# Kernel tuning notes

Hardware: AMD Instinct MI355X
Metric: run time of the kernel (lower is better)

Reference implementation:

```python
import jax, jax.numpy as jnp
import numpy as np

V, D, H, L, S, B, HD, FF, MAXS = 50257, 1024, 8, 6, 1024, 2, 128, 4096, 2048
EPS = 1e-5
STD = 0.02


def rmsnorm(x, w):
    rms = jnp.sqrt(jnp.mean(x * x, axis=-1, keepdims=True) + EPS)
    return w * (x / rms)


def setup_inputs() -> dict:
    key = jax.random.key(0)
    ks = jax.random.split(key, 9)
    return {
        "tokens": jax.random.randint(ks[0], (S, B), 0, V),
        "tok_emb": STD * jax.random.normal(ks[1], (V, D), jnp.float32),
        "pos_emb": STD * jax.random.normal(ks[2], (MAXS, D), jnp.float32),
        "attn_norm_w": jnp.ones((L, D), jnp.float32),
        "Wq": STD * jax.random.normal(ks[3], (L, H, D, HD), jnp.float32),
        "Wk": STD * jax.random.normal(ks[4], (L, H, D, HD), jnp.float32),
        "Wv": STD * jax.random.normal(ks[5], (L, H, D, HD), jnp.float32),
        "Wo": STD * jax.random.normal(ks[6], (L, H, HD, D), jnp.float32),
        "mlp_norm_w": jnp.ones((L, D), jnp.float32),
        "W1": STD * jax.random.normal(ks[7], (L, D, FF), jnp.float32),
        "W2": STD * jax.random.normal(ks[8], (L, FF, D), jnp.float32),
        "final_norm_w": jnp.ones((D,), jnp.float32),
    }


def reference(tokens, tok_emb, pos_emb, attn_norm_w, Wq, Wk, Wv, Wo,
              mlp_norm_w, W1, W2, final_norm_w):
    seq_len = tokens.shape[0]
    scale = HD ** -0.5
    # (S, B, D) token + learned positional embeddings
    x = tok_emb[tokens] + pos_emb[:seq_len][:, None, :]
    causal = jnp.tril(jnp.ones((seq_len, seq_len), bool))  # (S, S)
    for l in range(L):
        n = rmsnorm(x, attn_norm_w[l])
        q = jnp.einsum('sbd,hdk->bhsk', n, Wq[l])
        k = jnp.einsum('sbd,hdk->bhsk', n, Wk[l])
        v = jnp.einsum('sbd,hdk->bhsk', n, Wv[l])
        scores = jnp.einsum('bhsk,bhtk->bhst', q, k) * scale
        scores = jnp.where(causal, scores, -jnp.inf)
        w = jax.nn.softmax(scores, axis=-1)
        attn = jnp.einsum('bhst,bhtk->bhsk', w, v)
        # per-head out_proj summed over heads (matches sum over head modules)
        x = x + jnp.einsum('bhsk,hkd->sbd', attn, Wo[l])
        m = rmsnorm(x, mlp_norm_w[l])
        h = jax.nn.silu(jnp.einsum('sbd,df->sbf', m, W1[l]))
        x = x + jnp.einsum('sbf,fd->sbd', h, W2[l])
    x = rmsnorm(x, final_norm_w)
    logits = jnp.einsum('sbd,vd->sbv', x, tok_emb)  # tied lm_head
    return logits
```

## Files before the change

### kernel.cpp

```cpp
#include <hip/hip_runtime.h>
#include <hip/hip_bf16.h>
#include <cstddef>
#include <cstdint>

#define VOCAB 50257
#define VPAD  50432
#define DMODEL 1024
#define NHEAD 8
#define NLAYER 6
#define SEQ 1024
#define BATCH 2
#define HDIM 128
#define FFDIM 4096
#define NTOK (SEQ * BATCH)
#define QKVLD 3072
#define EPSV 1e-5f


typedef __attribute__((ext_vector_type(8))) short short8;
typedef __attribute__((ext_vector_type(4))) float f32x4;

__device__ __forceinline__ unsigned short f2bf(float f) {
    union { float f; unsigned u; } v; v.f = f;
    unsigned r = v.u + 0x7FFF + ((v.u >> 16) & 1);
    return (unsigned short)(r >> 16);
}

__global__ __launch_bounds__(256) void embed_kernel(
    const int* __restrict__ tokens, const float* __restrict__ tok_emb,
    const float* __restrict__ pos_emb, float* __restrict__ x)
{
    int idx = blockIdx.x * 256 + threadIdx.x;
    int t = idx >> 10;
    int d = idx & (DMODEL - 1);
    int b = t >> 10, s = t & (SEQ - 1);
    int tok = tokens[s * BATCH + b];
    x[idx] = tok_emb[(size_t)tok * DMODEL + d] + pos_emb[(size_t)s * DMODEL + d];
}

__global__ __launch_bounds__(256) void rmsnorm_bf_kernel(
    const float* __restrict__ x, const float* __restrict__ w,
    unsigned short* __restrict__ o)
{
    int t = blockIdx.x;
    int tid = threadIdx.x;
    const float4 xv = ((const float4*)(x + (size_t)t * DMODEL))[tid];
    float ss = xv.x * xv.x + xv.y * xv.y + xv.z * xv.z + xv.w * xv.w;
    __shared__ float red[256];
    red[tid] = ss;
    __syncthreads();
    for (int off = 128; off > 0; off >>= 1) {
        if (tid < off) red[tid] += red[tid + off];
        __syncthreads();
    }
    float inv = rsqrtf(red[0] * (1.0f / DMODEL) + EPSV);
    const float4 wv = ((const float4*)w)[tid];
    ushort4 ov;
    ov.x = f2bf(wv.x * xv.x * inv);
    ov.y = f2bf(wv.y * xv.y * inv);
    ov.z = f2bf(wv.z * xv.z * inv);
    ov.w = f2bf(wv.w * xv.w * inv);
    ((ushort4*)(o + (size_t)t * DMODEL))[tid] = ov;
}

__global__ __launch_bounds__(256) void transpose_cast_kernel(
    const float* __restrict__ in, unsigned short* __restrict__ out, int R, int C)
{
    __shared__ float tile[32][33];
    const size_t bo = (size_t)blockIdx.z * R * C;
    const float* src = in + bo;
    unsigned short* dst = out + bo;
    int c0 = blockIdx.x * 32, r0 = blockIdx.y * 32;
    int tx = threadIdx.x, ty = threadIdx.y;
    #pragma unroll
    for (int i = 0; i < 32; i += 8)
        tile[ty + i][tx] = src[(size_t)(r0 + ty + i) * C + c0 + tx];
    __syncthreads();
    #pragma unroll
    for (int i = 0; i < 32; i += 8)
        dst[(size_t)(c0 + ty + i) * R + r0 + tx] = f2bf(tile[tx][ty + i]);
}

__global__ __launch_bounds__(256) void transpose_qkv_kernel(
    const float* __restrict__ in, unsigned short* __restrict__ out, int row_off)
{
    __shared__ float tile[32][33];
    int z = blockIdx.z;
    int l = z >> 3, h = z & 7;
    const float* src = in + (size_t)z * DMODEL * HDIM;
    unsigned short* dst = out + (size_t)l * QKVLD * DMODEL
                              + (size_t)(row_off + h * HDIM) * DMODEL;
    int c0 = blockIdx.x * 32, r0 = blockIdx.y * 32;
    int tx = threadIdx.x, ty = threadIdx.y;
    #pragma unroll
    for (int i = 0; i < 32; i += 8)
        tile[ty + i][tx] = src[(size_t)(r0 + ty + i) * HDIM + c0 + tx];
    __syncthreads();
    #pragma unroll
    for (int i = 0; i < 32; i += 8)
        dst[(size_t)(c0 + ty + i) * DMODEL + r0 + tx] = f2bf(tile[tx][ty + i]);
}

__global__ __launch_bounds__(256) void vt_transpose_kernel(
    const unsigned short* __restrict__ qkv, unsigned short* __restrict__ vt)
{
    __shared__ unsigned short tile[32][33];
    int c0 = blockIdx.x * 32;
    int r0 = blockIdx.y * 32;
    int tx = threadIdx.x, ty = threadIdx.y;
    #pragma unroll
    for (int i = 0; i < 32; i += 8)
        tile[ty + i][tx] = qkv[(size_t)(r0 + ty + i) * QKVLD + 2048 + c0 + tx];
    __syncthreads();
    #pragma unroll
    for (int i = 0; i < 32; i += 8)
        vt[(size_t)(c0 + ty + i) * NTOK + r0 + tx] = tile[tx][ty + i];
}

__global__ __launch_bounds__(256) void cast_pad_kernel(
    const float* __restrict__ in, unsigned short* __restrict__ out,
    long n_src, long n_tot)
{
    long i = ((long)blockIdx.x * 256 + threadIdx.x) * 8;
    if (i >= n_tot) return;
    short8 o8;
    if (i < n_src) {
        const float4* p = (const float4*)(in + i);
        float4 a = p[0], b = p[1];
        o8[0] = (short)f2bf(a.x); o8[1] = (short)f2bf(a.y);
        o8[2] = (short)f2bf(a.z); o8[3] = (short)f2bf(a.w);
        o8[4] = (short)f2bf(b.x); o8[5] = (short)f2bf(b.y);
        o8[6] = (short)f2bf(b.z); o8[7] = (short)f2bf(b.w);
    } else {
        o8 = (short8)0;
    }
    *(short8*)(out + i) = o8;
}

template<bool ATOMIC, bool SILU, bool BF16OUT, int RM>
__global__ __launch_bounds__(256, 2) void mm128_kernel(
    const unsigned short* __restrict__ A, const unsigned short* __restrict__ Bt,
    void* __restrict__ Cv, int M, int N, int K, int rows, int ksplit)
{
    int nwg = gridDim.x;
    int flat = blockIdx.x;
    int q8 = nwg >> 3, r8 = nwg & 7;
    int xcd = flat & 7, lid = flat >> 3;
    int wg = (r8 == 0) ? (xcd * q8 + lid)
           : ((xcd < r8 ? xcd * (q8 + 1) : r8 * (q8 + 1) + (xcd - r8) * q8) + lid);
    int rs = rows * ksplit;
    const int col0 = (wg / rs) * 128;
    int rem = wg % rs;
    const int row0 = (rem / ksplit) * 128;
    const int sk   = rem % ksplit;
    const int Keff = K / ksplit;
    const int kbase = sk * Keff;

    __shared__ __align__(16) char lds[65536];
    const int tid  = threadIdx.x;
    const int lane = tid & 63;
    const int wave = tid >> 6;
    const int wm = wave >> 1, wn = wave & 1;
    const int g  = lane >> 4;
    const int c  = lane & 15;

    f32x4 acc[4][4] = {};

    auto STAGE = [&](int buf, int t) {
        const int k0 = kbase + t * 32;
        char* base = lds + buf * 16384;
        #pragma unroll
        for (int j = 0; j < 2; ++j) {
            int chunk = j * 256 + tid;
            int row = chunk >> 2, slot = chunk & 3;
            int ss = slot ^ ((row >> 1) & 3);
            __builtin_amdgcn_global_load_lds(
                (const __attribute__((address_space(1))) void*)
                    (A + (size_t)(row0 + row) * K + k0 + ss * 8),
                (__attribute__((address_space(3))) void*)(base + chunk * 16), 16, 0, 0);
        }
        #pragma unroll
        for (int j = 0; j < 2; ++j) {
            int chunk = j * 256 + tid;
            int row = chunk >> 2, slot = chunk & 3;
            int ss = slot ^ ((row >> 1) & 3);
            __builtin_amdgcn_global_load_lds(
                (const __attribute__((address_space(1))) void*)
                    (Bt + (size_t)(col0 + row) * K + k0 + ss * 8),
                (__attribute__((address_space(3))) void*)(base + 8192 + chunk * 16), 16, 0, 0);
        }
    };

    const int NT = Keff >> 5;
    STAGE(0, 0);
    if (NT > 1) STAGE(1, 1);
    if (NT > 2) STAGE(2, 2);
    if (NT > 2)      asm volatile("s_waitcnt vmcnt(8)" ::: "memory");
    else if (NT > 1) asm volatile("s_waitcnt vmcnt(4)" ::: "memory");
    else             asm volatile("s_waitcnt vmcnt(0)" ::: "memory");
    __builtin_amdgcn_s_barrier();
    __builtin_amdgcn_sched_barrier(0);

    for (int t = 0; t < NT; ++t) {
        if (t + 3 < NT) STAGE((t + 3) & 3, t + 3);

        char* base = lds + (t & 3) * 16384;
        short8 af[4], bf[4];
        #pragma unroll
        for (int i = 0; i < 4; ++i) {
            int rowa = wm * 64 + i * 16 + c;
            af[i] = *(const short8*)(base + rowa * 64 + ((g ^ ((rowa >> 1) & 3)) << 4));
            int rowb = wn * 64 + i * 16 + c;
            bf[i] = *(const short8*)(base + 8192 + rowb * 64 + ((g ^ ((rowb >> 1) & 3)) << 4));
        }
        __builtin_amdgcn_s_setprio(1);
        #pragma unroll
        for (int i = 0; i < 4; ++i)
            #pragma unroll
            for (int j = 0; j < 4; ++j)
                acc[i][j] = __builtin_amdgcn_mfma_f32_16x16x32_bf16(
                    af[i], bf[j], acc[i][j], 0, 0, 0);
        __builtin_amdgcn_s_setprio(0);
        __builtin_amdgcn_sched_barrier(0);

        if (t + 1 < NT) {
            if (t + 3 < NT)      asm volatile("s_waitcnt vmcnt(8)" ::: "memory");
            else if (t + 2 < NT) asm volatile("s_waitcnt vmcnt(4)" ::: "memory");
            else                 asm volatile("s_waitcnt vmcnt(0)" ::: "memory");
            __builtin_amdgcn_s_barrier();
            __builtin_amdgcn_sched_barrier(0);
        }
    }

    float* Cf = (float*)Cv;
    unsigned short* Cb = (unsigned short*)Cv;
    const int crow  = row0 + wm * 64 + g * 4;
    const int ccol0 = col0 + wn * 64 + c;
    #pragma unroll
    for (int i = 0; i < 4; ++i) {
        #pragma unroll
        for (int j = 0; j < 4; ++j) {
            int gcol = ccol0 + j * 16;
            if (gcol < N) {
                #pragma unroll
                for (int r = 0; r < 4; ++r) {
                    int grow = crow + i * 16 + r;
                    int orow = RM ? (((grow & (SEQ - 1)) << 1) | (grow >> 10)) : grow;
                    float v = acc[i][j][r];
                    if (SILU) v = v / (1.0f + __expf(-v));
                    size_t ci = (size_t)orow * N + gcol;
                    if (ATOMIC)       atomicAdd(&Cf[ci], v);
                    else if (BF16OUT) Cb[ci] = f2bf(v);
                    else              Cf[ci] = v;
                }
            }
        }
    }
}

template<bool SILU, bool BF16OUT, int RM>
__global__ __launch_bounds__(512, 1) void mm256_kernel(
    const unsigned short* __restrict__ A, const unsigned short* __restrict__ Bt,
    void* __restrict__ Cv, int M, int N, int K, int rows)
{
    int nwg = gridDim.x;
    int flat = blockIdx.x;
    int q8 = nwg >> 3, r8 = nwg & 7;
    int xcd = flat & 7, lid = flat >> 3;
    int wg = (r8 == 0) ? (xcd * q8 + lid)
           : ((xcd < r8 ? xcd * (q8 + 1) : r8 * (q8 + 1) + (xcd - r8) * q8) + lid);
    const int row0 = (wg % rows) * 256;
    const int col0 = (wg / rows) * 256;

    __shared__ __align__(16) char lds[131072];
    const int tid  = threadIdx.x;
    const int lane = tid & 63;
    const int wave = tid >> 6;
    const int wm = wave >> 2;
    const int wn = wave & 3;
    const int g  = lane >> 4;
    const int c  = lane & 15;

    f32x4 acc[8][4] = {};

    auto STAGE = [&](int buf, int tile) {
        const int k0 = tile * 32;
        char* base = lds + buf * 32768;
        #pragma unroll
        for (int j = 0; j < 2; ++j) {
            int chunk = j * 512 + tid;
            int row = chunk >> 2, slot = chunk & 3;
            int sslot = slot ^ ((row >> 1) & 3);
            __builtin_amdgcn_global_load_lds(
                (const __attribute__((address_space(1))) void*)
                    (A + (size_t)(row0 + row) * K + k0 + sslot * 8),
                (__attribute__((address_space(3))) void*)(base + chunk * 16), 16, 0, 0);
        }
        #pragma unroll
        for (int j = 0; j < 2; ++j) {
            int chunk = j * 512 + tid;
            int row = chunk >> 2, slot = chunk & 3;
            int sslot = slot ^ ((row >> 1) & 3);
            __builtin_amdgcn_global_load_lds(
                (const __attribute__((address_space(1))) void*)
                    (Bt + (size_t)(col0 + row) * K + k0 + sslot * 8),
                (__attribute__((address_space(3))) void*)(base + 16384 + chunk * 16), 16, 0, 0);
        }
    };

    const int NT = K >> 5;
    STAGE(0, 0); STAGE(1, 1); STAGE(2, 2);
    asm volatile("s_waitcnt vmcnt(8)" ::: "memory");
    __builtin_amdgcn_s_barrier();
    __builtin_amdgcn_sched_barrier(0);

    for (int t = 0; t < NT; ++t) {
        if (t + 3 < NT) STAGE((t + 3) & 3, t + 3);

        char* base = lds + (t & 3) * 32768;
        short8 af[8], bf[4];
        #pragma unroll
        for (int mf = 0; mf < 8; ++mf) {
            int row = wm * 128 + mf * 16 + c;
            af[mf] = *(const short8*)(base + row * 64 + ((g ^ ((row >> 1) & 3)) << 4));
        }
        #pragma unroll
        for (int nf = 0; nf < 4; ++nf) {
            int row = wn * 64 + nf * 16 + c;
            bf[nf] = *(const short8*)(base + 16384 + row * 64 + ((g ^ ((row >> 1) & 3)) << 4));
        }
        __builtin_amdgcn_s_setprio(1);
        #pragma unroll
        for (int mf = 0; mf < 8; ++mf)
            #pragma unroll
            for (int nf = 0; nf < 4; ++nf)
                acc[mf][nf] = __builtin_amdgcn_mfma_f32_16x16x32_bf16(
                    af[mf], bf[nf], acc[mf][nf], 0, 0, 0);
        __builtin_amdgcn_s_setprio(0);
        __builtin_amdgcn_sched_barrier(0);

        if (t + 1 < NT) {
            if (t + 3 < NT)      asm volatile("s_waitcnt vmcnt(8)" ::: "memory");
            else if (t + 2 < NT) asm volatile("s_waitcnt vmcnt(4)" ::: "memory");
            else                 asm volatile("s_waitcnt vmcnt(0)" ::: "memory");
            __builtin_amdgcn_s_barrier();
            __builtin_amdgcn_sched_barrier(0);
        }
    }

    float* Cf = (float*)Cv;
    unsigned short* Cb = (unsigned short*)Cv;
    #pragma unroll
    for (int mf = 0; mf < 8; ++mf) {
        #pragma unroll
        for (int nf = 0; nf < 4; ++nf) {
            int gcol = col0 + wn * 64 + nf * 16 + c;
            if (gcol < N) {
                #pragma unroll
                for (int r = 0; r < 4; ++r) {
                    int grow = row0 + wm * 128 + mf * 16 + g * 4 + r;
                    int orow = RM ? (((grow & (SEQ - 1)) << 1) | (grow >> 10)) : grow;
                    float v = acc[mf][nf][r];
                    if (SILU) v = v / (1.0f + __expf(-v));
                    size_t ci = (size_t)orow * N + gcol;
                    if (BF16OUT) Cb[ci] = f2bf(v);
                    else         Cf[ci] = v;
                }
            }
        }
    }
}

__global__ __launch_bounds__(256) void flash_attn_kernel(
    const unsigned short* __restrict__ q, const unsigned short* __restrict__ k,
    const unsigned short* __restrict__ vt, unsigned short* __restrict__ o)
{
    const int qt   = blockIdx.x;
    const int h    = blockIdx.y;
    const int b    = blockIdx.z;
    const int tid  = threadIdx.x;
    const int lane = tid & 63;
    const int wave = tid >> 6;
    const int g    = lane >> 4;
    const int c    = lane & 15;

    __shared__ unsigned short k_lds[64 * 128];
    __shared__ unsigned short vt_lds[128 * 64];
    __shared__ unsigned short p_lds[4 * 16 * 64];

    const int q0  = qt * 64;
    const int wq0 = q0 + wave * 16;
    const int tokb = b * SEQ;

    short8 qf[4];
    {
        const unsigned short* qr =
            q + (size_t)(tokb + wq0 + c) * QKVLD + h * HDIM + g * 8;
        #pragma unroll
        for (int dblk = 0; dblk < 4; ++dblk)
            qf[dblk] = *(const short8*)(qr + dblk * 32);
    }

    f32x4 oacc[8] = {};
    float m = -1e30f, l = 0.f;
    const float scale = 0.08838834764831845f;
    const int myq = wq0 + c;

    const int nt = qt + 1;
    for (int it = 0; it < nt; ++it) {
        const int kv0 = it * 64;
        short8 kc[4], vc[4];
        #pragma unroll
        for (int i = 0; i < 4; ++i) {
            int chunk = tid + i * 256;
            int key = chunk >> 4, cc = chunk & 15;
            kc[i] = *(const short8*)(
                k + (size_t)(tokb + kv0 + key) * QKVLD + h * HDIM + cc * 8);
        }
        #pragma unroll
        for (int i = 0; i < 4; ++i) {
            int chunk = tid + i * 256;
            int d = chunk >> 3, cc = chunk & 7;
            vc[i] = *(const short8*)(
                vt + (size_t)(h * HDIM + d) * NTOK + tokb + kv0 + cc * 8);
        }
        __syncthreads();
        #pragma unroll
        for (int i = 0; i < 4; ++i) {
            int chunk = tid + i * 256;
            int key = chunk >> 4, cc = chunk & 15;
            *(short8*)((char*)k_lds + ((key * 256 + cc * 16) ^ ((key & 7) << 4))) = kc[i];
        }
        #pragma unroll
        for (int i = 0; i < 4; ++i) {
            int chunk = tid + i * 256;
            int d = chunk >> 3, cc = chunk & 7;
            *(short8*)((char*)vt_lds + ((d * 128 + cc * 16) ^ ((d & 7) << 4))) = vc[i];
        }
        __syncthreads();

        f32x4 st[4];
        #pragma unroll
        for (int sub = 0; sub < 4; ++sub) {
            f32x4 acc = {};
            int key = sub * 16 + c;
            #pragma unroll
            for (int dblk = 0; dblk < 4; ++dblk) {
                short8 kf = *(const short8*)((char*)k_lds +
                    ((key * 256 + dblk * 64 + g * 16) ^ ((key & 7) << 4)));
                acc = __builtin_amdgcn_mfma_f32_16x16x32_bf16(kf, qf[dblk], acc, 0, 0, 0);
            }
            st[sub] = acc;
        }

        #pragma unroll
        for (int sub = 0; sub < 4; ++sub)
            #pragma unroll
            for (int r = 0; r < 4; ++r) {
                int key = kv0 + sub * 16 + g * 4 + r;
                float s = st[sub][r] * scale;
                st[sub][r] = (key <= myq) ? s : -1e30f;
            }

        float tm = -1e30f;
        #pragma unroll
        for (int sub = 0; sub < 4; ++sub)
            #pragma unroll
            for (int r = 0; r < 4; ++r) tm = fmaxf(tm, st[sub][r]);
        tm = fmaxf(tm, __shfl_xor(tm, 16));
        tm = fmaxf(tm, __shfl_xor(tm, 32));
        float mnew = fmaxf(m, tm);
        float sc_f = __expf(m - mnew);
        m = mnew;

        float ps = 0.f;
        #pragma unroll
        for (int sub = 0; sub < 4; ++sub) {
            float p0 = __expf(st[sub][0] - m);
            float p1 = __expf(st[sub][1] - m);
            float p2 = __expf(st[sub][2] - m);
            float p3 = __expf(st[sub][3] - m);
            ps += (p0 + p1) + (p2 + p3);
            ushort4 pk;
            pk.x = f2bf(p0); pk.y = f2bf(p1); pk.z = f2bf(p2); pk.w = f2bf(p3);
            *(ushort4*)((char*)p_lds + wave * 2048 +
                ((c * 128 + sub * 32 + g * 8) ^ ((c & 7) << 4))) = pk;
        }
        ps += __shfl_xor(ps, 16);
        ps += __shfl_xor(ps, 32);
        l = l * sc_f + ps;
        #pragma unroll
        for (int dt = 0; dt < 8; ++dt)
            #pragma unroll
            for (int r = 0; r < 4; ++r) oacc[dt][r] *= sc_f;

        #pragma unroll
        for (int kb = 0; kb < 2; ++kb) {
            short8 pf = *(const short8*)((char*)p_lds + wave * 2048 +
                ((c * 128 + kb * 64 + g * 16) ^ ((c & 7) << 4)));
            #pragma unroll
            for (int dt = 0; dt < 8; ++dt) {
                int d = dt * 16 + c;
                short8 vf = *(const short8*)((char*)vt_lds +
                    ((d * 128 + kb * 64 + g * 16) ^ ((d & 7) << 4)));
                oacc[dt] = __builtin_amdgcn_mfma_f32_16x16x32_bf16(vf, pf, oacc[dt], 0, 0, 0);
            }
        }
    }

    float inv = 1.0f / l;
    unsigned short* orow = o + (size_t)(tokb + wq0 + c) * DMODEL + h * HDIM + g * 4;
    #pragma unroll
    for (int dt = 0; dt < 8; ++dt) {
        ushort4 ov;
        ov.x = f2bf(oacc[dt][0] * inv);
        ov.y = f2bf(oacc[dt][1] * inv);
        ov.z = f2bf(oacc[dt][2] * inv);
        ov.w = f2bf(oacc[dt][3] * inv);
        *(ushort4*)(orow + dt * 16) = ov;
    }
}

extern "C" void kernel_launch(void* const* d_in, const int* in_sizes, int n_in,
                              void* d_out, int out_size, void* d_ws, size_t ws_size,
                              hipStream_t stream)
{
    const int*   tokens       = (const int*)  d_in[0];
    const float* tok_emb      = (const float*)d_in[1];
    const float* pos_emb      = (const float*)d_in[2];
    const float* attn_norm_w  = (const float*)d_in[3];
    const float* Wq           = (const float*)d_in[4];
    const float* Wk           = (const float*)d_in[5];
    const float* Wv           = (const float*)d_in[6];
    const float* Wo           = (const float*)d_in[7];
    const float* mlp_norm_w   = (const float*)d_in[8];
    const float* W1           = (const float*)d_in[9];
    const float* W2           = (const float*)d_in[10];
    const float* final_norm_w = (const float*)d_in[11];
    float* out = (float*)d_out;

    char* wp = (char*)d_ws;
    size_t off = 0;
    auto alloc = [&](size_t bytes) -> void* {
        void* p = wp + off;
        off += (bytes + 255) & ~(size_t)255;
        return p;
    };
    float* x             = (float*)alloc((size_t)NTOK * DMODEL * 4);
    unsigned short* nbf     = (unsigned short*)alloc((size_t)NTOK * DMODEL * 2);
    unsigned short* qkvbf   = (unsigned short*)alloc((size_t)NTOK * QKVLD * 2);
    unsigned short* vtb     = (unsigned short*)alloc((size_t)DMODEL * NTOK * 2);
    unsigned short* attnbf  = (unsigned short*)alloc((size_t)NTOK * DMODEL * 2);
    unsigned short* hbf     = (unsigned short*)alloc((size_t)NTOK * FFDIM * 2);
    unsigned short* temb    = (unsigned short*)alloc((size_t)VPAD * DMODEL * 2);
    unsigned short* Wqkv_t  = (unsigned short*)alloc((size_t)NLAYER * QKVLD * DMODEL * 2);
    unsigned short* Wo_t    = (unsigned short*)alloc((size_t)NLAYER * DMODEL * DMODEL * 2);
    unsigned short* W1_t    = (unsigned short*)alloc((size_t)NLAYER * DMODEL * FFDIM * 2);
    unsigned short* W2_t    = (unsigned short*)alloc((size_t)NLAYER * FFDIM * DMODEL * 2);
    if (off > ws_size) return;

    {
        dim3 bb(32, 8), g(HDIM / 32, DMODEL / 32, NLAYER * NHEAD);
        transpose_qkv_kernel<<<g, bb, 0, stream>>>(Wq, Wqkv_t, 0);
        transpose_qkv_kernel<<<g, bb, 0, stream>>>(Wk, Wqkv_t, DMODEL);
        transpose_qkv_kernel<<<g, bb, 0, stream>>>(Wv, Wqkv_t, 2 * DMODEL);
    }
    {
        dim3 bb(32, 8), g(DMODEL / 32, DMODEL / 32, NLAYER);
        transpose_cast_kernel<<<g, bb, 0, stream>>>(Wo, Wo_t, DMODEL, DMODEL);
    }
    {
        dim3 bb(32, 8), g(FFDIM / 32, DMODEL / 32, NLAYER);
        transpose_cast_kernel<<<g, bb, 0, stream>>>(W1, W1_t, DMODEL, FFDIM);
    }
    {
        dim3 bb(32, 8), g(DMODEL / 32, FFDIM / 32, NLAYER);
        transpose_cast_kernel<<<g, bb, 0, stream>>>(W2, W2_t, FFDIM, DMODEL);
    }
    {
        long n_src = (long)VOCAB * DMODEL, n_tot = (long)VPAD * DMODEL;
        cast_pad_kernel<<<(unsigned)(n_tot / 8 / 256), 256, 0, stream>>>(
            tok_emb, temb, n_src, n_tot);
    }

    embed_kernel<<<(NTOK * DMODEL) / 256, 256, 0, stream>>>(tokens, tok_emb, pos_emb, x);

    const size_t LW    = (size_t)DMODEL * DMODEL;
    const size_t LWQKV = (size_t)QKVLD * DMODEL;
    const size_t LWF   = (size_t)DMODEL * FFDIM;

    for (int l = 0; l < NLAYER; l++) {
        rmsnorm_bf_kernel<<<NTOK, 256, 0, stream>>>(x, attn_norm_w + (size_t)l * DMODEL, nbf);
        mm128_kernel<false, false, true, 0><<<384, 256, 0, stream>>>(
            nbf, Wqkv_t + l * LWQKV, qkvbf, NTOK, QKVLD, DMODEL, 16, 1);
        vt_transpose_kernel<<<dim3(DMODEL / 32, NTOK / 32), dim3(32, 8), 0, stream>>>(
            qkvbf, vtb);
        flash_attn_kernel<<<dim3(SEQ / 64, NHEAD, BATCH), 256, 0, stream>>>(
            qkvbf, qkvbf + DMODEL, vtb, attnbf);
        mm128_kernel<true, false, false, 0><<<8 * 16 * 2, 256, 0, stream>>>(
            attnbf, Wo_t + l * LW, x, NTOK, DMODEL, DMODEL, 16, 2);
        rmsnorm_bf_kernel<<<NTOK, 256, 0, stream>>>(x, mlp_norm_w + (size_t)l * DMODEL, nbf);
        mm128_kernel<false, true, true, 0><<<32 * 16, 256, 0, stream>>>(
            nbf, W1_t + l * LWF, hbf, NTOK, FFDIM, DMODEL, 16, 1);
        mm128_kernel<true, false, false, 0><<<8 * 16 * 2, 256, 0, stream>>>(
            hbf, W2_t + l * LWF, x, NTOK, DMODEL, FFDIM, 16, 2);
    }

    rmsnorm_bf_kernel<<<NTOK, 256, 0, stream>>>(x, final_norm_w, nbf);
    mm256_kernel<false, false, 1><<<8 * 197, 512, 0, stream>>>(
        nbf, temb, out, NTOK, VOCAB, DMODEL, 8);
}
```

Measured before the change: 1.415 ms.

## Restructure lm_head GEMM into ping-pong half-tile staging pipeline

Rewrites the 256x256 lm_head GEMM main loop to use 64-wide K tiles split into four quarter-stages with two LDS buffers. Each global-to-LDS load for an operand half is issued between MFMA sub-blocks, and barriers are placed around each compute phase. The goal is to interleave memory loads more finely with matrix math and to read fewer fragments into registers at a time. The cost is more barriers per iteration and a more intricate wait-count schedule, which risks stalls or races if the counts are wrong.

After: 1.427 ms. Within noise of the previous version (+0.9%).

```diff
diff --git a/kernel.cpp b/kernel.cpp
--- a/kernel.cpp
+++ b/kernel.cpp
@@ -259,7 +259,7 @@
 }
 
 template<bool SILU, bool BF16OUT, int RM>
-__global__ __launch_bounds__(512, 1) void mm256_kernel(
+__global__ __launch_bounds__(512, 1) void mm256p_kernel(
     const unsigned short* __restrict__ A, const unsigned short* __restrict__ Bt,
     void* __restrict__ Cv, int M, int N, int K, int rows)
 {
@@ -283,69 +283,104 @@
 
     f32x4 acc[8][4] = {};
 
-    auto STAGE = [&](int buf, int tile) {
-        const int k0 = tile * 32;
-        char* base = lds + buf * 32768;
+    auto STAGE = [&](int buf, int op, int ks, int tile) {
+        char* base = lds + (buf << 16) + (op << 15) + (ks << 14);
+        const unsigned short* src =
+            (op ? Bt + (size_t)col0 * K : A + (size_t)row0 * K) + tile * 64 + ks * 32;
         #pragma unroll
         for (int j = 0; j < 2; ++j) {
             int chunk = j * 512 + tid;
             int row = chunk >> 2, slot = chunk & 3;
-            int sslot = slot ^ ((row >> 1) & 3);
+            int ss = slot ^ ((row >> 1) & 3);
             __builtin_amdgcn_global_load_lds(
                 (const __attribute__((address_space(1))) void*)
-                    (A + (size_t)(row0 + row) * K + k0 + sslot * 8),
+                    (src + (size_t)row * K + ss * 8),
                 (__attribute__((address_space(3))) void*)(base + chunk * 16), 16, 0, 0);
         }
-        #pragma unroll
-        for (int j = 0; j < 2; ++j) {
-            int chunk = j * 512 + tid;
-            int row = chunk >> 2, slot = chunk & 3;
-            int sslot = slot ^ ((row >> 1) & 3);
-            __builtin_amdgcn_global_load_lds(
-                (const __attribute__((address_space(1))) void*)
-                    (Bt + (size_t)(col0 + row) * K + k0 + sslot * 8),
-                (__attribute__((address_space(3))) void*)(base + 16384 + chunk * 16), 16, 0, 0);
-        }
     };
-
-    const int NT = K >> 5;
-    STAGE(0, 0); STAGE(1, 1); STAGE(2, 2);
-    asm volatile("s_waitcnt vmcnt(8)" ::: "memory");
+    auto RD = [&](int buf, int op, int ks, int row) -> short8 {
+        char* base = lds + (buf << 16) + (op << 15) + (ks << 14);
+        return *(const short8*)(base + row * 64 + ((g ^ ((row >> 1) & 3)) << 4));
+    };
+
+    const int NT = K >> 6;
+    STAGE(0, 1, 0, 0); STAGE(0, 0, 0, 0); STAGE(0, 1, 1, 0); STAGE(0, 0, 1, 0);
+    STAGE(1, 1, 0, 1); STAGE(1, 0, 0, 1); STAGE(1, 1, 1, 1);
+    asm volatile("s_waitcnt vmcnt(6)" ::: "memory");
     __builtin_amdgcn_s_barrier();
     __builtin_amdgcn_sched_barrier(0);
 
-    for (int t = 0; t < NT; ++t) {
-        if (t + 3 < NT) STAGE((t + 3) & 3, t + 3);
-
-        char* base = lds + (t & 3) * 32768;
-        short8 af[8], bf[4];
-        #pragma unroll
-        for (int mf = 0; mf < 8; ++mf) {
-            int row = wm * 128 + mf * 16 + c;
-            af[mf] = *(const short8*)(base + row * 64 + ((g ^ ((row >> 1) & 3)) << 4));
-        }
-        #pragma unroll
-        for (int nf = 0; nf < 4; ++nf) {
-            int row = wn * 64 + nf * 16 + c;
-            bf[nf] = *(const short8*)(base + 16384 + row * 64 + ((g ^ ((row >> 1) & 3)) << 4));
-        }
+    for (int T = 0; T < NT; ++T) {
+        const int buf = T & 1;
+        short8 af[4], bf[4];
+
+        #pragma unroll
+        for (int i = 0; i < 4; ++i) af[i] = RD(buf, 0, 0, wm * 128 + i * 16 + c);
+        #pragma unroll
+        for (int j = 0; j < 4; ++j) bf[j] = RD(buf, 1, 0, wn * 64 + j * 16 + c);
+        if (T + 1 < NT) STAGE(buf ^ 1, 0, 1, T + 1);
+        __builtin_amdgcn_s_barrier();
         __builtin_amdgcn_s_setprio(1);
         #pragma unroll
-        for (int mf = 0; mf < 8; ++mf)
-            #pragma unroll
-            for (int nf = 0; nf < 4; ++nf)
-                acc[mf][nf] = __builtin_amdgcn_mfma_f32_16x16x32_bf16(
-                    af[mf], bf[nf], acc[mf][nf], 0, 0, 0);
+        for (int i = 0; i < 4; ++i)
+            #pragma unroll
+            for (int j = 0; j < 4; ++j)
+                acc[i][j] = __builtin_amdgcn_mfma_f32_16x16x32_bf16(
+                    af[i], bf[j], acc[i][j], 0, 0, 0);
         __builtin_amdgcn_s_setprio(0);
+        __builtin_amdgcn_s_barrier();
         __builtin_amdgcn_sched_barrier(0);
 
-        if (t + 1 < NT) {
-            if (t + 3 < NT)      asm volatile("s_waitcnt vmcnt(8)" ::: "memory");
-            else if (t + 2 < NT) asm volatile("s_waitcnt vmcnt(4)" ::: "memory");
-            else                 asm volatile("s_waitcnt vmcnt(0)" ::: "memory");
+        #pragma unroll
+        for (int i = 0; i < 4; ++i) af[i] = RD(buf, 0, 0, wm * 128 + 64 + i * 16 + c);
+        if (T + 2 < NT) STAGE(buf, 1, 0, T + 2);
+        __builtin_amdgcn_s_barrier();
+        __builtin_amdgcn_s_setprio(1);
+        #pragma unroll
+        for (int i = 0; i < 4; ++i)
+            #pragma unroll
+            for (int j = 0; j < 4; ++j)
+                acc[4 + i][j] = __builtin_amdgcn_mfma_f32_16x16x32_bf16(
+                    af[i], bf[j], acc[4 + i][j], 0, 0, 0);
+        __builtin_amdgcn_s_setprio(0);
+        __builtin_amdgcn_s_barrier();
+        __builtin_amdgcn_sched_barrier(0);
+
+        #pragma unroll
+        for (int i = 0; i < 4; ++i) af[i] = RD(buf, 0, 1, wm * 128 + i * 16 + c);
+        #pragma unroll
+        for (int j = 0; j < 4; ++j) bf[j] = RD(buf, 1, 1, wn * 64 + j * 16 + c);
+        if (T + 2 < NT) STAGE(buf, 0, 0, T + 2);
+        __builtin_amdgcn_s_barrier();
+        __builtin_amdgcn_s_setprio(1);
+        #pragma unroll
+        for (int i = 0; i < 4; ++i)
+            #pragma unroll
+            for (int j = 0; j < 4; ++j)
+                acc[i][j] = __builtin_amdgcn_mfma_f32_16x16x32_bf16(
+                    af[i], bf[j], acc[i][j], 0, 0, 0);
+        __builtin_amdgcn_s_setprio(0);
+        __builtin_amdgcn_s_barrier();
+        __builtin_amdgcn_sched_barrier(0);
+
+        #pragma unroll
+        for (int i = 0; i < 4; ++i) af[i] = RD(buf, 0, 1, wm * 128 + 64 + i * 16 + c);
+        if (T + 2 < NT) STAGE(buf, 1, 1, T + 2);
+        __builtin_amdgcn_s_barrier();
+        __builtin_amdgcn_s_setprio(1);
+        #pragma unroll
+        for (int i = 0; i < 4; ++i)
+            #pragma unroll
+            for (int j = 0; j < 4; ++j)
+                acc[4 + i][j] = __builtin_amdgcn_mfma_f32_16x16x32_bf16(
+                    af[i], bf[j], acc[4 + i][j], 0, 0, 0);
+        __builtin_amdgcn_s_setprio(0);
+        if (T + 1 < NT) {
+            if (T + 2 < NT) asm volatile("s_waitcnt vmcnt(6)" ::: "memory");
+            else            asm volatile("s_waitcnt vmcnt(0)" ::: "memory");
             __builtin_amdgcn_s_barrier();
-            __builtin_amdgcn_sched_barrier(0);
-        }
+        }
+        __builtin_amdgcn_sched_barrier(0);
     }
 
     float* Cf = (float*)Cv;
@@ -607,6 +642,6 @@
     }
 
     rmsnorm_bf_kernel<<<NTOK, 256, 0, stream>>>(x, final_norm_w, nbf);
-    mm256_kernel<false, false, 1><<<8 * 197, 512, 0, stream>>>(
+    mm256p_kernel<false, false, 1><<<8 * 197, 512, 0, stream>>>(
         nbf, temb, out, NTOK, VOCAB, DMODEL, 8);
 }
```

## Fuse V-transpose into QKV GEMM epilogue and use wave-per-row RMSNorm

Applied to the files above, without the earlier changes.

The QKV projection GEMM now writes the V columns straight into the transposed V buffer from its epilogue, which removes the separate vt_transpose kernel launch and its extra read and write of V. RMSNorm is rewritten so each wavefront handles one token row and reduces with cross-lane shuffles instead of an LDS tree with repeated barriers. The transposed V stores are strided by NTOK and uncoalesced, so the GEMM epilogue may get slower. Both changes are small next to the GEMMs and attention.

Result: slower. 1.458 ms (+3.1%).

```diff
diff --git a/kernel.cpp b/kernel.cpp
--- a/kernel.cpp
+++ b/kernel.cpp
@@ -42,25 +42,32 @@
     const float* __restrict__ x, const float* __restrict__ w,
     unsigned short* __restrict__ o)
 {
-    int t = blockIdx.x;
-    int tid = threadIdx.x;
-    const float4 xv = ((const float4*)(x + (size_t)t * DMODEL))[tid];
-    float ss = xv.x * xv.x + xv.y * xv.y + xv.z * xv.z + xv.w * xv.w;
-    __shared__ float red[256];
-    red[tid] = ss;
-    __syncthreads();
-    for (int off = 128; off > 0; off >>= 1) {
-        if (tid < off) red[tid] += red[tid + off];
-        __syncthreads();
-    }
-    float inv = rsqrtf(red[0] * (1.0f / DMODEL) + EPSV);
-    const float4 wv = ((const float4*)w)[tid];
-    ushort4 ov;
-    ov.x = f2bf(wv.x * xv.x * inv);
-    ov.y = f2bf(wv.y * xv.y * inv);
-    ov.z = f2bf(wv.z * xv.z * inv);
-    ov.w = f2bf(wv.w * xv.w * inv);
-    ((ushort4*)(o + (size_t)t * DMODEL))[tid] = ov;
+    const int wave = threadIdx.x >> 6, lane = threadIdx.x & 63;
+    const int t = blockIdx.x * 4 + wave;
+    const float4* xr = (const float4*)(x + (size_t)t * DMODEL);
+    const float4* wr = (const float4*)w;
+    float4 xv[4];
+    float ss = 0.f;
+    #pragma unroll
+    for (int j = 0; j < 4; ++j) {
+        xv[j] = xr[lane + 64 * j];
+        ss += xv[j].x * xv[j].x + xv[j].y * xv[j].y
+            + xv[j].z * xv[j].z + xv[j].w * xv[j].w;
+    }
+    #pragma unroll
+    for (int off = 1; off < 64; off <<= 1) ss += __shfl_xor(ss, off);
+    float inv = rsqrtf(ss * (1.0f / DMODEL) + EPSV);
+    ushort4* orow = (ushort4*)(o + (size_t)t * DMODEL);
+    #pragma unroll
+    for (int j = 0; j < 4; ++j) {
+        float4 wv = wr[lane + 64 * j];
+        ushort4 ov;
+        ov.x = f2bf(wv.x * xv[j].x * inv);
+        ov.y = f2bf(wv.y * xv[j].y * inv);
+        ov.z = f2bf(wv.z * xv[j].z * inv);
+        ov.w = f2bf(wv.w * xv[j].w * inv);
+        orow[lane + 64 * j] = ov;
+    }
 }
 
 __global__ __launch_bounds__(256) void transpose_cast_kernel(
@@ -99,22 +106,6 @@
     #pragma unroll
     for (int i = 0; i < 32; i += 8)
         dst[(size_t)(c0 + ty + i) * DMODEL + r0 + tx] = f2bf(tile[tx][ty + i]);
-}
-
-__global__ __launch_bounds__(256) void vt_transpose_kernel(
-    const unsigned short* __restrict__ qkv, unsigned short* __restrict__ vt)
-{
-    __shared__ unsigned short tile[32][33];
-    int c0 = blockIdx.x * 32;
-    int r0 = blockIdx.y * 32;
-    int tx = threadIdx.x, ty = threadIdx.y;
-    #pragma unroll
-    for (int i = 0; i < 32; i += 8)
-        tile[ty + i][tx] = qkv[(size_t)(r0 + ty + i) * QKVLD + 2048 + c0 + tx];
-    __syncthreads();
-    #pragma unroll
-    for (int i = 0; i < 32; i += 8)
-        vt[(size_t)(c0 + ty + i) * NTOK + r0 + tx] = tile[tx][ty + i];
 }
 
 __global__ __launch_bounds__(256) void cast_pad_kernel(
@@ -137,10 +128,11 @@
     *(short8*)(out + i) = o8;
 }
 
-template<bool ATOMIC, bool SILU, bool BF16OUT, int RM>
+template<bool ATOMIC, bool SILU, bool BF16OUT, int RM, int VT>
 __global__ __launch_bounds__(256, 2) void mm128_kernel(
     const unsigned short* __restrict__ A, const unsigned short* __restrict__ Bt,
-    void* __restrict__ Cv, int M, int N, int K, int rows, int ksplit)
+    void* __restrict__ Cv, unsigned short* __restrict__ Vt,
+    int M, int N, int K, int rows, int ksplit)
 {
     int nwg = gridDim.x;
     int flat = blockIdx.x;
@@ -248,10 +240,14 @@
                     int orow = RM ? (((grow & (SEQ - 1)) << 1) | (grow >> 10)) : grow;
                     float v = acc[i][j][r];
                     if (SILU) v = v / (1.0f + __expf(-v));
-                    size_t ci = (size_t)orow * N + gcol;
-                    if (ATOMIC)       atomicAdd(&Cf[ci], v);
-                    else if (BF16OUT) Cb[ci] = f2bf(v);
-                    else              Cf[ci] = v;
+                    if (VT && gcol >= 2048) {
+                        Vt[(size_t)(gcol - 2048) * NTOK + grow] = f2bf(v);
+                    } else {
+                        size_t ci = (size_t)orow * N + gcol;
+                        if (ATOMIC)       atomicAdd(&Cf[ci], v);
+                        else if (BF16OUT) Cb[ci] = f2bf(v);
+                        else              Cf[ci] = v;
+                    }
                 }
             }
         }
@@ -590,23 +586,23 @@
     const size_t LWF   = (size_t)DMODEL * FFDIM;
 
     for (int l = 0; l < NLAYER; l++) {
-        rmsnorm_bf_kernel<<<NTOK, 256, 0, stream>>>(x, attn_norm_w + (size_t)l * DMODEL, nbf);
-        mm128_kernel<false, false, true, 0><<<384, 256, 0, stream>>>(
-            nbf, Wqkv_t + l * LWQKV, qkvbf, NTOK, QKVLD, DMODEL, 16, 1);
-        vt_transpose_kernel<<<dim3(DMODEL / 32, NTOK / 32), dim3(32, 8), 0, stream>>>(
-            qkvbf, vtb);
+        rmsnorm_bf_kernel<<<NTOK / 4, 256, 0, stream>>>(
+            x, attn_norm_w + (size_t)l * DMODEL, nbf);
+        mm128_kernel<false, false, true, 0, 1><<<384, 256, 0, stream>>>(
+            nbf, Wqkv_t + l * LWQKV, qkvbf, vtb, NTOK, QKVLD, DMODEL, 16, 1);
         flash_attn_kernel<<<dim3(SEQ / 64, NHEAD, BATCH), 256, 0, stream>>>(
             qkvbf, qkvbf + DMODEL, vtb, attnbf);
-        mm128_kernel<true, false, false, 0><<<8 * 16 * 2, 256, 0, stream>>>(
-            attnbf, Wo_t + l * LW, x, NTOK, DMODEL, DMODEL, 16, 2);
-        rmsnorm_bf_kernel<<<NTOK, 256, 0, stream>>>(x, mlp_norm_w + (size_t)l * DMODEL, nbf);
-        mm128_kernel<false, true, true, 0><<<32 * 16, 256, 0, stream>>>(
-            nbf, W1_t + l * LWF, hbf, NTOK, FFDIM, DMODEL, 16, 1);
-        mm128_kernel<true, false, false, 0><<<8 * 16 * 2, 256, 0, stream>>>(
-            hbf, W2_t + l * LWF, x, NTOK, DMODEL, FFDIM, 16, 2);
-    }
-
-    rmsnorm_bf_kernel<<<NTOK, 256, 0, stream>>>(x, final_norm_w, nbf);
+        mm128_kernel<true, false, false, 0, 0><<<8 * 16 * 2, 256, 0, stream>>>(
+            attnbf, Wo_t + l * LW, x, nullptr, NTOK, DMODEL, DMODEL, 16, 2);
+        rmsnorm_bf_kernel<<<NTOK / 4, 256, 0, stream>>>(
+            x, mlp_norm_w + (size_t)l * DMODEL, nbf);
+        mm128_kernel<false, true, true, 0, 0><<<32 * 16, 256, 0, stream>>>(
+            nbf, W1_t + l * LWF, hbf, nullptr, NTOK, FFDIM, DMODEL, 16, 1);
+        mm128_kernel<true, false, false, 0, 0><<<8 * 16 * 2, 256, 0, stream>>>(
+            hbf, W2_t + l * LWF, x, nullptr, NTOK, DMODEL, FFDIM, 16, 2);
+    }
+
+    rmsnorm_bf_kernel<<<NTOK / 4, 256, 0, stream>>>(x, final_norm_w, nbf);
     mm256_kernel<false, false, 1><<<8 * 197, 512, 0, stream>>>(
         nbf, temb, out, NTOK, VOCAB, DMODEL, 8);
 }
```
